# Kernel tuning notes

Hardware: AMD Instinct MI355X
Metric: run time of the kernel (lower is better)

## Reference

```python
import jax, jax.numpy as jnp
import numpy as np

N0, N1, N2 = 100000, 50000, 10000
E1, E2 = 1600000, 320000
D = 128


def setup_inputs() -> dict:
    key = jax.random.key(0)
    ks = jax.random.split(key, 9)
    return {
        "x": jax.random.normal(ks[0], (N0, D), dtype=jnp.float32),
        "ew1": jax.random.uniform(ks[1], (E1,), dtype=jnp.float32),
        "ew2": jax.random.uniform(ks[2], (E2,), dtype=jnp.float32),
        "W": jax.random.normal(ks[3], (D, D), dtype=jnp.float32) * (1.0 / np.sqrt(D)),
        "b": jax.random.normal(ks[4], (D,), dtype=jnp.float32) * 0.01,
        "e1_src": jax.random.randint(ks[5], (E1,), 0, N0),
        "e1_dst": jax.random.randint(ks[6], (E1,), 0, N1),
        "e2_src": jax.random.randint(ks[7], (E2,), 0, N1),
        "e2_dst": jax.random.randint(ks[8], (E2,), 0, N2),
    }


def _spmm_block(h, src, dst, ew, num_dst):
    # u_mul_e + sum: m_e = h[src_e] * ew_e, reduced by sum onto dst nodes
    msgs = h[src] * ew[:, None]  # [E, D]
    return jax.ops.segment_sum(msgs, dst, num_segments=num_dst)


def reference(x, ew1, ew2, W, b, e1_src, e1_dst, e2_src, e2_dst):
    h = _spmm_block(x, e1_src, e1_dst, ew1, N1)   # block 1: [N1, D]
    h = _spmm_block(h, e2_src, e2_dst, ew2, N2)   # block 2: [N2, D]
    return h @ W.T + b                            # Linear(emb_dim, emb_dim)
```

## Files before the change

kernel.cpp:

```cpp
#include <hip/hip_runtime.h>

#define DD 128

constexpr int cN0 = 100000, cN1 = 50000, cN2 = 10000;
constexpr int NB1c = (cN1 + 31) / 32;
constexpr int NB2c = (cN2 + 15) / 16;
constexpr int CAP1 = 2048;
constexpr int CAP2 = 1024;

typedef unsigned long long ull;

__device__ __forceinline__ float bf_lo(unsigned int u) {
  return __uint_as_float(u << 16);
}
__device__ __forceinline__ float bf_hi(unsigned int u) {
  return __uint_as_float(u & 0xFFFF0000u);
}
__device__ __forceinline__ unsigned int pack_bf2(float a, float b) {
  unsigned int ua = __float_as_uint(a), ub = __float_as_uint(b);
  ua += 0x7FFFu + ((ua >> 16) & 1u);
  ub += 0x7FFFu + ((ub >> 16) & 1u);
  return (ua >> 16) | (ub & 0xFFFF0000u);
}

#define PAY_GATHER(PK, VX, VY)                                       \
  {                                                                  \
    int s_ = ((int)(unsigned int)(PK)) >> 5;                         \
    unsigned int v_ = h_in[(size_t)s_ * 64 + lane];                  \
    float w_ = __uint_as_float((unsigned int)((PK) >> 32));          \
    VX += bf_lo(v_) * w_;                                            \
    VY += bf_hi(v_) * w_;                                            \
  }

__global__ __launch_bounds__(256) void cvt_bf16_kernel(
    const float* __restrict__ in, unsigned int* __restrict__ outp, long long n8) {
  long long i = (long long)blockIdx.x * 256 + threadIdx.x;
  if (i >= n8) return;
  const float4* f4 = reinterpret_cast<const float4*>(in) + i * 2;
  float4 a = f4[0];
  float4 b = f4[1];
  uint4 o;
  o.x = pack_bf2(a.x, a.y);
  o.y = pack_bf2(a.z, a.w);
  o.z = pack_bf2(b.x, b.y);
  o.w = pack_bf2(b.z, b.w);
  reinterpret_cast<uint4*>(outp)[i] = o;
}

__global__ __launch_bounds__(256) void wt_kernel(
    const float* __restrict__ W, float* __restrict__ WT) {
  int idx = blockIdx.x * 256 + threadIdx.x;
  int c = idx >> 7;
  int d = idx & 127;
  WT[d * DD + c] = W[idx];
}

__global__ __launch_bounds__(1024) void passA_kernel(
    const int* __restrict__ d1, int E1, int nA1, int* __restrict__ bh1, int nblk1,
    const int* __restrict__ d2, int E2, int* __restrict__ bh2, int nblk2) {
  __shared__ int hist[NB1c];
  int lb = blockIdx.x;
  const int* dst; int E, NB, nblk, sh; int* bh;
  if (lb < nA1) { dst = d1; E = E1; NB = NB1c; nblk = nblk1; bh = bh1; sh = 5; }
  else { lb -= nA1; dst = d2; E = E2; NB = NB2c; nblk = nblk2; bh = bh2; sh = 4; }

  int t = threadIdx.x;
  for (int i = t; i < NB; i += 1024) hist[i] = 0;
  __syncthreads();

  int eb = lb * 4096;
#pragma unroll
  for (int r = 0; r < 4; ++r) {
    int e = eb + r * 1024 + t;
    if (e < E) atomicAdd(&hist[dst[e] >> sh], 1);
  }
  __syncthreads();
  for (int i = t; i < NB; i += 1024) bh[(size_t)i * nblk + lb] = hist[i];
}

__global__ __launch_bounds__(256) void scan_blk2_kernel(
    const int* __restrict__ cnt1, int n1, int* __restrict__ ofs1, int* __restrict__ bsum1, int nb1,
    const int* __restrict__ cnt2, int n2, int* __restrict__ ofs2, int* __restrict__ bsum2) {
  const int* cnt; int n; int* ofs; int* bsum; int lb;
  if ((int)blockIdx.x < nb1) { cnt = cnt1; n = n1; ofs = ofs1; bsum = bsum1; lb = blockIdx.x; }
  else                       { cnt = cnt2; n = n2; ofs = ofs2; bsum = bsum2; lb = blockIdx.x - nb1; }

  __shared__ int tsum[256];
  int t = threadIdx.x;
  int base = lb * 4096 + t * 16;
  bool in = (base + 16 <= n);

  int v[16];
  if (in) {
    const int4* p4 = reinterpret_cast<const int4*>(cnt + base);
    int4 a = p4[0], b = p4[1], c = p4[2], d = p4[3];
    v[0]=a.x; v[1]=a.y; v[2]=a.z; v[3]=a.w;
    v[4]=b.x; v[5]=b.y; v[6]=b.z; v[7]=b.w;
    v[8]=c.x; v[9]=c.y; v[10]=c.z; v[11]=c.w;
    v[12]=d.x; v[13]=d.y; v[14]=d.z; v[15]=d.w;
  } else {
#pragma unroll
    for (int k = 0; k < 16; ++k) v[k] = 0;
  }
#pragma unroll
  for (int k = 1; k < 16; ++k) v[k] += v[k - 1];

  tsum[t] = v[15];
  __syncthreads();
  for (int d_ = 1; d_ < 256; d_ <<= 1) {
    int x = (t >= d_) ? tsum[t - d_] : 0;
    __syncthreads();
    tsum[t] += x;
    __syncthreads();
  }
  int ex = (t == 0) ? 0 : tsum[t - 1];

  if (in) {
    int4* q = reinterpret_cast<int4*>(ofs + base);
    q[0] = make_int4(ex,         ex + v[0],  ex + v[1],  ex + v[2]);
    q[1] = make_int4(ex + v[3],  ex + v[4],  ex + v[5],  ex + v[6]);
    q[2] = make_int4(ex + v[7],  ex + v[8],  ex + v[9],  ex + v[10]);
    q[3] = make_int4(ex + v[11], ex + v[12], ex + v[13], ex + v[14]);
  }
  if (t == 255) bsum[lb] = tsum[255];
}

__global__ __launch_bounds__(1024) void scan_bsum2_kernel(
    int* __restrict__ bsum1, int nb1, int* __restrict__ bsum2, int nb2) {
  int* bsum; int nb;
  if (blockIdx.x == 0) { bsum = bsum1; nb = nb1; }
  else                 { bsum = bsum2; nb = nb2; }

  __shared__ int part[1024];
  int t = threadIdx.x;
  int orig = (t < nb) ? bsum[t] : 0;
  part[t] = orig;
  __syncthreads();
  for (int d_ = 1; d_ < 1024; d_ <<= 1) {
    int x = (t >= d_) ? part[t - d_] : 0;
    __syncthreads();
    part[t] += x;
    __syncthreads();
  }
  if (t < nb) bsum[t] = part[t] - orig;
}

__global__ __launch_bounds__(1024) void passB_kernel(
    const int* __restrict__ d1, const int* __restrict__ s1, const float* __restrict__ w1,
    int E1, int nA1, const int* __restrict__ S1, const int* __restrict__ bs1,
    int nblk1, ull* __restrict__ coarse1,
    const int* __restrict__ d2, const int* __restrict__ s2, const float* __restrict__ w2,
    int E2, const int* __restrict__ S2, const int* __restrict__ bs2,
    int nblk2, ull* __restrict__ coarse2) {
  __shared__ int cnt[NB1c];
  int lb = blockIdx.x;
  const int* dst; const int* src; const float* ew;
  int E, NB, nblk, sh, msk; const int* S; const int* bs; ull* coarse;
  if (lb < nA1) {
    dst = d1; src = s1; ew = w1; E = E1; NB = NB1c; nblk = nblk1;
    S = S1; bs = bs1; coarse = coarse1; sh = 5; msk = 31;
  } else {
    lb -= nA1;
    dst = d2; src = s2; ew = w2; E = E2; NB = NB2c; nblk = nblk2;
    S = S2; bs = bs2; coarse = coarse2; sh = 4; msk = 15;
  }

  int t = threadIdx.x;
  for (int i = t; i < NB; i += 1024) cnt[i] = 0;
  __syncthreads();

  int eb = lb * 4096;
#pragma unroll
  for (int r = 0; r < 4; ++r) {
    int e = eb + r * 1024 + t;
    if (e < E) {
      int d_ = dst[e];
      int bkt = d_ >> sh;
      int rk = atomicAdd(&cnt[bkt], 1);
      size_t idx = (size_t)bkt * nblk + lb;
      int pos = S[idx] + bs[idx >> 12] + rk;
      ull pk = ((ull)__float_as_uint(ew[e]) << 32) |
               (unsigned int)((src[e] << 5) | (d_ & msk));
      __builtin_nontemporal_store(pk, coarse + pos);
    }
  }
}

__global__ __launch_bounds__(256) void bucket_spmm1_kernel(
    const unsigned int* __restrict__ h_in,
    const int* __restrict__ S, const int* __restrict__ bs, int nblk,
    const ull* __restrict__ coarse, int E,
    unsigned int* __restrict__ h1b) {
  __shared__ ull pay[CAP1];
  __shared__ int h32[32], c32[32], binofs[32];
  int b = blockIdx.x;
  int t = threadIdx.x;
  int wid = t >> 6, lane = t & 63;

  size_t i0 = (size_t)b * nblk;
  int base = S[i0] + bs[i0 >> 12];
  int end;
  if (b == NB1c - 1) end = E;
  else {
    size_t i1 = (size_t)(b + 1) * nblk;
    end = S[i1] + bs[i1 >> 12];
  }
  int count = end - base;

  if (count <= CAP1) {
    if (t < 32) { h32[t] = 0; c32[t] = 0; }
    __syncthreads();
    for (int i = base + t; i < end; i += 256)
      atomicAdd(&h32[(int)(unsigned int)coarse[i] & 31], 1);
    __syncthreads();
    if (t == 0) {
      int run = 0;
#pragma unroll
      for (int k = 0; k < 32; ++k) { binofs[k] = run; run += h32[k]; }
    }
    __syncthreads();
    for (int i = base + t; i < end; i += 256) {
      ull pk = coarse[i];
      int dl = (int)(unsigned int)pk & 31;
      int rk = atomicAdd(&c32[dl], 1);
      pay[binofs[dl] + rk] = pk;
    }
    __syncthreads();

#pragma unroll
    for (int r = 0; r < 8; ++r) {
      int dl = wid * 8 + r;
      int row = b * 32 + dl;
      if (row >= cN1) break;
      int lo = binofs[dl], hi = lo + h32[dl];
      float accx = 0.f, accy = 0.f, ax1 = 0.f, ay1 = 0.f;
      int j = lo;
      for (; j + 8 <= hi; j += 8) {
        ull p0 = pay[j],     p1 = pay[j + 1], p2 = pay[j + 2], p3 = pay[j + 3];
        ull p4 = pay[j + 4], p5 = pay[j + 5], p6 = pay[j + 6], p7 = pay[j + 7];
        PAY_GATHER(p0, accx, accy) PAY_GATHER(p1, ax1, ay1)
        PAY_GATHER(p2, accx, accy) PAY_GATHER(p3, ax1, ay1)
        PAY_GATHER(p4, accx, accy) PAY_GATHER(p5, ax1, ay1)
        PAY_GATHER(p6, accx, accy) PAY_GATHER(p7, ax1, ay1)
      }
      for (; j < hi; ++j) { ull p0 = pay[j]; PAY_GATHER(p0, accx, accy) }
      h1b[(size_t)row * 64 + lane] = pack_bf2(accx + ax1, accy + ay1);
    }
  } else {
    for (int r = 0; r < 8; ++r) {
      int dl = wid * 8 + r;
      int row = b * 32 + dl;
      if (row >= cN1) break;
      float accx = 0.f, accy = 0.f;
      for (int i = base; i < end; ++i) {
        ull pk = coarse[i];
        if (((int)(unsigned int)pk & 31) == dl) { PAY_GATHER(pk, accx, accy) }
      }
      h1b[(size_t)row * 64 + lane] = pack_bf2(accx, accy);
    }
  }
}

__global__ __launch_bounds__(256) void bucket_spmm2_linear_kernel(
    const unsigned int* __restrict__ h_in,
    const int* __restrict__ S, const int* __restrict__ bs, int nblk,
    const ull* __restrict__ coarse, int E,
    const float* __restrict__ WT,
    const float* __restrict__ bias,
    float* __restrict__ out) {
  __shared__ ull pay[CAP2];
  __shared__ float hrow[16][DD];
  __shared__ int h16[16], c16[16], binofs[16];
  int b = blockIdx.x;
  int t = threadIdx.x;
  int wid = t >> 6, lane = t & 63;

  size_t i0 = (size_t)b * nblk;
  int base = S[i0] + bs[i0 >> 12];
  int end;
  if (b == NB2c - 1) end = E;
  else {
    size_t i1 = (size_t)(b + 1) * nblk;
    end = S[i1] + bs[i1 >> 12];
  }
  int count = end - base;

  if (count <= CAP2) {
    if (t < 16) { h16[t] = 0; c16[t] = 0; }
    __syncthreads();
    for (int i = base + t; i < end; i += 256)
      atomicAdd(&h16[(int)(unsigned int)coarse[i] & 15], 1);
    __syncthreads();
    if (t == 0) {
      int run = 0;
#pragma unroll
      for (int k = 0; k < 16; ++k) { binofs[k] = run; run += h16[k]; }
    }
    __syncthreads();
    for (int i = base + t; i < end; i += 256) {
      ull pk = coarse[i];
      int dl = (int)(unsigned int)pk & 15;
      int rk = atomicAdd(&c16[dl], 1);
      pay[binofs[dl] + rk] = pk;
    }
    __syncthreads();

#pragma unroll
    for (int r = 0; r < 4; ++r) {
      int dl = wid * 4 + r;
      int lo = binofs[dl], hi = lo + h16[dl];
      float accx = 0.f, accy = 0.f, ax1 = 0.f, ay1 = 0.f;
      int j = lo;
      for (; j + 8 <= hi; j += 8) {
        ull p0 = pay[j],     p1 = pay[j + 1], p2 = pay[j + 2], p3 = pay[j + 3];
        ull p4 = pay[j + 4], p5 = pay[j + 5], p6 = pay[j + 6], p7 = pay[j + 7];
        PAY_GATHER(p0, accx, accy) PAY_GATHER(p1, ax1, ay1)
        PAY_GATHER(p2, accx, accy) PAY_GATHER(p3, ax1, ay1)
        PAY_GATHER(p4, accx, accy) PAY_GATHER(p5, ax1, ay1)
        PAY_GATHER(p6, accx, accy) PAY_GATHER(p7, ax1, ay1)
      }
      for (; j < hi; ++j) { ull p0 = pay[j]; PAY_GATHER(p0, accx, accy) }
      float2 hv; hv.x = accx + ax1; hv.y = accy + ay1;
      *reinterpret_cast<float2*>(&hrow[dl][2 * lane]) = hv;
    }
  } else {
    for (int r = 0; r < 4; ++r) {
      int dl = wid * 4 + r;
      float accx = 0.f, accy = 0.f;
      for (int i = base; i < end; ++i) {
        ull pk = coarse[i];
        if (((int)(unsigned int)pk & 15) == dl) { PAY_GATHER(pk, accx, accy) }
      }
      float2 hv; hv.x = accx; hv.y = accy;
      *reinterpret_cast<float2*>(&hrow[dl][2 * lane]) = hv;
    }
  }

  float2 bb = reinterpret_cast<const float2*>(bias)[lane];
  float a0[4], a1[4];
#pragma unroll
  for (int r = 0; r < 4; ++r) { a0[r] = bb.x; a1[r] = bb.y; }

  const float* hbase = &hrow[wid * 4][0];
#pragma unroll 4
  for (int d = 0; d < DD; ++d) {
    float2 wv = *reinterpret_cast<const float2*>(WT + (size_t)d * DD + 2 * lane);
#pragma unroll
    for (int r = 0; r < 4; ++r) {
      float h = hbase[r * DD + d];
      a0[r] += h * wv.x;
      a1[r] += h * wv.y;
    }
  }
#pragma unroll
  for (int r = 0; r < 4; ++r) {
    int row = b * 16 + wid * 4 + r;
    if (row < cN2) {
      float2 o; o.x = a0[r]; o.y = a1[r];
      reinterpret_cast<float2*>(out + (size_t)row * DD)[lane] = o;
    }
  }
}

static inline size_t align256(size_t x) { return (x + 255) & ~size_t(255); }
static inline int pad16i(int x) { return (x + 15) & ~15; }

extern "C" void kernel_launch(void* const* d_in, const int* in_sizes, int n_in,
                              void* d_out, int out_size, void* d_ws, size_t ws_size,
                              hipStream_t stream) {
  const float* x   = (const float*)d_in[0];
  const float* ew1 = (const float*)d_in[1];
  const float* ew2 = (const float*)d_in[2];
  const float* W   = (const float*)d_in[3];
  const float* b   = (const float*)d_in[4];
  const int* e1_src = (const int*)d_in[5];
  const int* e1_dst = (const int*)d_in[6];
  const int* e2_src = (const int*)d_in[7];
  const int* e2_dst = (const int*)d_in[8];
  float* out = (float*)d_out;

  int E1 = in_sizes[1];
  int E2 = in_sizes[2];

  int nA1 = (E1 + 4095) / 4096;
  int nA2 = (E2 + 4095) / 4096;
  int nc1 = pad16i(NB1c * nA1);
  int nc2 = pad16i(NB2c * nA2);
  int nbs1 = (nc1 + 4095) / 4096;
  int nbs2 = (nc2 + 4095) / 4096;

  char* p = (char*)d_ws;
  unsigned int* xb  = (unsigned int*)p;  p += align256((size_t)cN0 * DD * 2);
  unsigned int* h1b = (unsigned int*)p;  p += align256((size_t)cN1 * DD * 2);
  float* WT = (float*)p;                 p += align256((size_t)DD * DD * 4);
  int* bh1 = (int*)p;                    p += align256((size_t)(nc1 + 16) * 4);
  int* bh2 = (int*)p;                    p += align256((size_t)(nc2 + 16) * 4);
  int* S1  = (int*)p;                    p += align256((size_t)(nc1 + 16) * 4);
  int* S2  = (int*)p;                    p += align256((size_t)(nc2 + 16) * 4);
  int* bsum1 = (int*)p;                  p += align256(4096);
  int* bsum2 = (int*)p;                  p += align256(4096);
  ull* coarse1 = (ull*)p;                p += align256((size_t)E1 * 8);
  ull* coarse2 = (ull*)p;                p += align256((size_t)E2 * 8);

  {
    long long n8 = (long long)cN0 * DD / 8;
    cvt_bf16_kernel<<<(int)((n8 + 255) / 256), 256, 0, stream>>>(x, xb, n8);
  }
  wt_kernel<<<64, 256, 0, stream>>>(W, WT);

  passA_kernel<<<nA1 + nA2, 1024, 0, stream>>>(
      e1_dst, E1, nA1, bh1, nA1, e2_dst, E2, bh2, nA2);

  scan_blk2_kernel<<<nbs1 + nbs2, 256, 0, stream>>>(
      bh1, nc1, S1, bsum1, nbs1, bh2, nc2, S2, bsum2);
  scan_bsum2_kernel<<<2, 1024, 0, stream>>>(bsum1, nbs1, bsum2, nbs2);

  passB_kernel<<<nA1 + nA2, 1024, 0, stream>>>(
      e1_dst, e1_src, ew1, E1, nA1, S1, bsum1, nA1, coarse1,
      e2_dst, e2_src, ew2, E2, S2, bsum2, nA2, coarse2);

  bucket_spmm1_kernel<<<NB1c, 256, 0, stream>>>(
      xb, S1, bsum1, nA1, coarse1, E1, h1b);

  bucket_spmm2_linear_kernel<<<NB2c, 256, 0, stream>>>(
      h1b, S2, bsum2, nA2, coarse2, E2, WT, b, out);
}
```

Baseline: 179.5 us.

## Stage bucket scatter through LDS so global payload writes become contiguous

The partition pass now first counts bucket sizes per block, runs a block-local exclusive scan, and places each packed edge into a shared-memory staging buffer sorted by bucket. Consecutive threads then write consecutive sorted entries to their global bucket cells, replacing random per-edge scattered stores with mostly contiguous runs. This adds a 1024-wide scan with many barriers, more LDS use (about 50KB), and a second pass of atomics, which may lower occupancy.

After: 151.3 us. 1.19x faster.

```diff
diff --git a/kernel.cpp b/kernel.cpp
--- a/kernel.cpp
+++ b/kernel.cpp
@@ -153,6 +153,12 @@
     int E2, const int* __restrict__ S2, const int* __restrict__ bs2,
     int nblk2, ull* __restrict__ coarse2) {
   __shared__ int cnt[NB1c];
+  __shared__ int lscan[NB1c];
+  __shared__ int cellst[NB1c];
+  __shared__ int part[1024];
+  __shared__ ull pay[4096];
+  __shared__ unsigned short bkt_of[4096];
+
   int lb = blockIdx.x;
   const int* dst; const int* src; const float* ew;
   int E, NB, nblk, sh, msk; const int* S; const int* bs; ull* coarse;
@@ -166,22 +172,69 @@
   }
 
   int t = threadIdx.x;
+  int eb = lb * 4096;
+  int ecount = E - eb; if (ecount > 4096) ecount = 4096;
+
   for (int i = t; i < NB; i += 1024) cnt[i] = 0;
   __syncthreads();
 
-  int eb = lb * 4096;
+  ull pk0 = 0, pk1 = 0, pk2 = 0, pk3 = 0;
+  int bk0 = -1, bk1 = -1, bk2 = -1, bk3 = -1;
+#define LOADE(R, PK, BK)                                              \
+  {                                                                   \
+    int e = eb + (R) * 1024 + t;                                      \
+    if (e < E) {                                                      \
+      int d_ = dst[e];                                                \
+      BK = d_ >> sh;                                                  \
+      PK = ((ull)__float_as_uint(ew[e]) << 32) |                      \
+           (unsigned int)((src[e] << 5) | (d_ & msk));                \
+      atomicAdd(&cnt[BK], 1);                                         \
+    }                                                                 \
+  }
+  LOADE(0, pk0, bk0) LOADE(1, pk1, bk1) LOADE(2, pk2, bk2) LOADE(3, pk3, bk3)
+#undef LOADE
+  __syncthreads();
+
+  int i0 = 2 * t, i1 = 2 * t + 1;
+  int c0 = (i0 < NB) ? cnt[i0] : 0;
+  int c1 = (i1 < NB) ? cnt[i1] : 0;
+  part[t] = c0 + c1;
+  __syncthreads();
+  for (int d_ = 1; d_ < 1024; d_ <<= 1) {
+    int x = (t >= d_) ? part[t - d_] : 0;
+    __syncthreads();
+    part[t] += x;
+    __syncthreads();
+  }
+  int ex = (t == 0) ? 0 : part[t - 1];
+  if (i0 < NB) lscan[i0] = ex;
+  if (i1 < NB) lscan[i1] = ex + c0;
+  __syncthreads();
+
+  for (int i = t; i < NB; i += 1024) {
+    size_t idx = (size_t)i * nblk + lb;
+    cellst[i] = S[idx] + bs[idx >> 12];
+    cnt[i] = lscan[i];
+  }
+  __syncthreads();
+
+#define PLACE(PK, BK)                                                 \
+  if (BK >= 0) {                                                      \
+    int pos = atomicAdd(&cnt[BK], 1);                                 \
+    pay[pos] = PK;                                                    \
+    bkt_of[pos] = (unsigned short)(BK);                               \
+  }
+  PLACE(pk0, bk0) PLACE(pk1, bk1) PLACE(pk2, bk2) PLACE(pk3, bk3)
+#undef PLACE
+  __syncthreads();
+
 #pragma unroll
   for (int r = 0; r < 4; ++r) {
-    int e = eb + r * 1024 + t;
-    if (e < E) {
-      int d_ = dst[e];
-      int bkt = d_ >> sh;
-      int rk = atomicAdd(&cnt[bkt], 1);
-      size_t idx = (size_t)bkt * nblk + lb;
-      int pos = S[idx] + bs[idx >> 12] + rk;
-      ull pk = ((ull)__float_as_uint(ew[e]) << 32) |
-               (unsigned int)((src[e] << 5) | (d_ & msk));
-      __builtin_nontemporal_store(pk, coarse + pos);
+    int p = r * 1024 + t;
+    if (p < ecount) {
+      int b_ = bkt_of[p];
+      int addr = cellst[b_] + (p - lscan[b_]);
+      __builtin_nontemporal_store(pay[p], coarse + addr);
     }
   }
 }
```
